# Performance work log

Hardware: AMD Instinct MI355X
Metric: run time of the kernel (lower is better)

## Reference

```python
import jax, jax.numpy as jnp
import numpy as np

N_ATOMS = 512
N_FEATURES = 64
BATCH = 8
BINS = 64
SEG_LEN = 1
LEAKY_SLOPE = 0.01


def _segments(n, length=1):
    # all pairs of segments (i,i+length),(j,j+length), i<j, excluding end1==start2
    n_seg = n - length
    i, j = np.triu_indices(n_seg, k=1)
    seg = np.stack([i, i + length, j, j + length], axis=1)
    return seg[seg[:, 1] != seg[:, 2]].astype(np.int32)


def _nnorm(v):
    return v / jnp.linalg.norm(v, axis=-1, keepdims=True)


def _writhe(segments, xyz):
    # segments: (P,4) int, xyz: (B,N,3) -> (B,P)
    smat = xyz[:, segments]                                  # (B,P,4,3)
    B, P = smat.shape[0], smat.shape[1]
    # displacements r02,r03,r12,r13 (point a in seg1 -> point b in seg2)
    disp = _nnorm((smat[:, :, None, 2:, :] - smat[:, :, :2, None, :]).reshape(B, P, 4, 3))
    idx_a = jnp.array([0, 1, 3, 2])
    idx_b = jnp.array([1, 3, 2, 0])
    crosses = _nnorm(jnp.cross(disp[:, :, idx_a], disp[:, :, idx_b]))
    dots = jnp.clip(jnp.sum(crosses * crosses[:, :, idx_b], axis=-1), -1.0, 1.0)
    omega = jnp.arcsin(dots).sum(-1)                         # (B,P)
    signs = jnp.sign(jnp.sum(
        jnp.cross(_nnorm(smat[:, :, 3] - smat[:, :, 2]), _nnorm(smat[:, :, 1] - smat[:, :, 0]))
        * disp[:, :, 0], axis=-1))
    return omega * signs / (2.0 * jnp.pi)


def _rbf(x, start=-1.0, end=1.0, number=BINS):
    # soft_one_hot_linspace, basis='gaussian', cutoff=False
    values = jnp.linspace(start, end, number, dtype=x.dtype)
    step = values[1] - values[0]
    diff = (x[..., None] - values) / step
    return jnp.exp(-(diff ** 2)) / 1.12


def setup_inputs() -> dict:
    key = jax.random.key(0)
    k = jax.random.split(key, 4)
    seg = jnp.asarray(_segments(N_ATOMS, SEG_LEN))           # (129795,4)
    return {
        "x": jax.random.normal(k[0], (BATCH, N_ATOMS, N_FEATURES), jnp.float32),
        "xyz": jax.random.normal(k[1], (BATCH, N_ATOMS, 3), jnp.float32) * 3.0,
        "segments": seg,
        "W1": jax.random.normal(k[2], (BINS, N_FEATURES), jnp.float32) / np.sqrt(BINS),
        "b1": jnp.zeros((N_FEATURES,), jnp.float32),
        "W2": jax.random.normal(k[3], (N_FEATURES, N_FEATURES), jnp.float32) / np.sqrt(N_FEATURES),
        "b2": jnp.zeros((N_FEATURES,), jnp.float32),
    }


def reference(x, xyz, segments, W1, b1, W2, b2):
    wr = _writhe(segments, xyz)                              # (B,P)
    # bidirectional edges between segment start points
    src = jnp.concatenate([segments[:, 0], segments[:, 2]])  # (E,)
    dst = jnp.concatenate([segments[:, 2], segments[:, 0]])  # (E,)
    wr_e = jnp.concatenate([wr, wr], axis=1)                 # (B,E)
    h = jax.nn.leaky_relu(_rbf(wr_e) @ W1 + b1, LEAKY_SLOPE) # (B,E,F)
    msg = (h @ W2 + b2) * x[:, src]                          # (B,E,F)
    agg = jax.vmap(lambda m: jax.ops.segment_sum(m, dst, num_segments=N_ATOMS))(msg)
    return x + agg                                           # residual update (B,N,F)
```

## Files before the change

### kernel.cpp

```cpp
#include <hip/hip_runtime.h>
#include <hip/hip_bf16.h>
#include <math.h>
#include <stdint.h>

#define N_ATOMS 512
#define NF 64
#define NB 8
#define NBINS 64
#define NSEG 511
#define NTF 8192
#define NSENT 2554
#define ETILES2 254

__device__ __forceinline__ float dot3(float ax, float ay, float az,
                                      float bx, float by, float bz) {
    return fmaf(ax, bx, fmaf(ay, by, az * bz));
}

__device__ __forceinline__ uint16_t bf16_bits(float f) {
    union { __hip_bfloat16 h; uint16_t u; } cv;
    cv.h = __float2bfloat16(f);
    return cv.u;
}

__device__ __forceinline__ float compute_wr(const float* pb, int i, int j) {
    float p0x = pb[3*i+0], p0y = pb[3*i+1], p0z = pb[3*i+2];
    float p1x = pb[3*i+3], p1y = pb[3*i+4], p1z = pb[3*i+5];
    float p2x = pb[3*j+0], p2y = pb[3*j+1], p2z = pb[3*j+2];
    float p3x = pb[3*j+3], p3y = pb[3*j+4], p3z = pb[3*j+5];

    float d0x = p2x-p0x, d0y = p2y-p0y, d0z = p2z-p0z;
    float d1x = p3x-p0x, d1y = p3y-p0y, d1z = p3z-p0z;
    float d2x = p2x-p1x, d2y = p2y-p1y, d2z = p2z-p1z;
    float d3x = p3x-p1x, d3y = p3y-p1y, d3z = p3z-p1z;
    {
        float n0 = rsqrtf(dot3(d0x,d0y,d0z,d0x,d0y,d0z)); d0x*=n0; d0y*=n0; d0z*=n0;
        float n1 = rsqrtf(dot3(d1x,d1y,d1z,d1x,d1y,d1z)); d1x*=n1; d1y*=n1; d1z*=n1;
        float n2 = rsqrtf(dot3(d2x,d2y,d2z,d2x,d2y,d2z)); d2x*=n2; d2y*=n2; d2z*=n2;
        float n3 = rsqrtf(dot3(d3x,d3y,d3z,d3x,d3y,d3z)); d3x*=n3; d3y*=n3; d3z*=n3;
    }
    float c0x = d0y*d1z - d0z*d1y, c0y = d0z*d1x - d0x*d1z, c0z = d0x*d1y - d0y*d1x;
    float c1x = d1y*d3z - d1z*d3y, c1y = d1z*d3x - d1x*d3z, c1z = d1x*d3y - d1y*d3x;
    float c3x = d2y*d0z - d2z*d0y, c3y = d2z*d0x - d2x*d0z, c3z = d2x*d0y - d2y*d0x;
    {
        float n0 = rsqrtf(dot3(c0x,c0y,c0z,c0x,c0y,c0z)); c0x*=n0; c0y*=n0; c0z*=n0;
        float n1 = rsqrtf(dot3(c1x,c1y,c1z,c1x,c1y,c1z)); c1x*=n1; c1y*=n1; c1z*=n1;
        float n3 = rsqrtf(dot3(c3x,c3y,c3z,c3x,c3y,c3z)); c3x*=n3; c3y*=n3; c3z*=n3;
    }
    float t0 = fminf(fmaxf(dot3(c0x,c0y,c0z, c1x,c1y,c1z), -1.f), 1.f);
    float t1 = fminf(fmaxf(dot3(c1x,c1y,c1z, c3x,c3y,c3z), -1.f), 1.f);
    float t3 = fminf(fmaxf(dot3(c3x,c3y,c3z, c0x,c0y,c0z), -1.f), 1.f);
    float omega = asinf(t0) + asinf(t1) + asinf(t3) + 1.5707963267948966f;
    float ex = p3x-p2x, ey = p3y-p2y, ez = p3z-p2z;
    float fx = p1x-p0x, fy = p1y-p0y, fz = p1z-p0z;
    float gx = ey*fz - ez*fy, gy = ez*fx - ex*fz, gz = ex*fy - ey*fx;
    float sgd = dot3(gx,gy,gz, d0x,d0y,d0z);
    float sgn = (sgd > 0.f) ? 1.f : ((sgd < 0.f) ? -1.f : 0.f);
    return omega * sgn * 0.15915494309189535f;
}

__device__ __forceinline__ uint32_t wr_to_off(float w) {
    float tf = (w + 1.0f) * ((float)(NTF - 1) * 0.5f);
    tf = fminf(fmaxf(tf, 0.0f), (float)(NTF - 1));
    int t0 = (int)(tf + 0.5f);
    t0 = (t0 > NTF - 1) ? (NTF - 1) : t0;
    return (uint32_t)t0 << 6;
}

__launch_bounds__(256)
__global__ void prepass(
        const float* __restrict__ xyz, const int* __restrict__ seg,
        const float* __restrict__ W1, const float* __restrict__ b1,
        const float* __restrict__ W2, const float* __restrict__ b2,
        uint16_t* __restrict__ tabh, uint32_t* __restrict__ ta, int P) {
    __shared__ float lds[1536];

    const unsigned bx = blockIdx.x;

    if (bx < NTF / 8) {
        const int widx = threadIdx.x >> 6;
        const int lane = threadIdx.x & 63;
        const int g = bx * 4 + widx;
        const int g2 = g + NTF / 2;

        float tta = ((-1.0f + (2.0f / (float)(NTF - 1)) * (float)g)  + 1.0f) * 31.5f;
        float ttb = ((-1.0f + (2.0f / (float)(NTF - 1)) * (float)g2) + 1.0f) * 31.5f;

        float a0=0.f,a1=0.f,a2=0.f,a3=0.f, e0=0.f,e1=0.f,e2=0.f,e3=0.f;
        #pragma unroll
        for (int k = 0; k < NBINS; k += 4) {
            #pragma unroll
            for (int q = 0; q < 4; ++q) {
                float da = tta - (float)(k + q);
                float db = ttb - (float)(k + q);
                float ra = __expf(-da * da) * 0.8928571428571429f;
                float rb = __expf(-db * db) * 0.8928571428571429f;
                float wv = W1[(k + q) * NF + lane];
                if (q == 0) { a0 = fmaf(ra, wv, a0); e0 = fmaf(rb, wv, e0); }
                if (q == 1) { a1 = fmaf(ra, wv, a1); e1 = fmaf(rb, wv, e1); }
                if (q == 2) { a2 = fmaf(ra, wv, a2); e2 = fmaf(rb, wv, e2); }
                if (q == 3) { a3 = fmaf(ra, wv, a3); e3 = fmaf(rb, wv, e3); }
            }
        }
        float ha = ((a0 + a1) + (a2 + a3)) + b1[lane];
        float hb = ((e0 + e1) + (e2 + e3)) + b1[lane];
        ha = fmaxf(ha, 0.01f * ha);
        hb = fmaxf(hb, 0.01f * hb);
        lds[widx * 64 + lane]       = ha;
        lds[256 + widx * 64 + lane] = hb;
        __syncthreads();

        float m0=0.f,m1=0.f,m2=0.f,m3=0.f, n0=0.f,n1=0.f,n2=0.f,n3=0.f;
        #pragma unroll
        for (int k = 0; k < NF; k += 4) {
            float w0 = W2[(k + 0) * NF + lane];
            float w1v = W2[(k + 1) * NF + lane];
            float w2v = W2[(k + 2) * NF + lane];
            float w3 = W2[(k + 3) * NF + lane];
            m0 = fmaf(lds[widx * 64 + k + 0], w0, m0);
            m1 = fmaf(lds[widx * 64 + k + 1], w1v, m1);
            m2 = fmaf(lds[widx * 64 + k + 2], w2v, m2);
            m3 = fmaf(lds[widx * 64 + k + 3], w3, m3);
            n0 = fmaf(lds[256 + widx * 64 + k + 0], w0, n0);
            n1 = fmaf(lds[256 + widx * 64 + k + 1], w1v, n1);
            n2 = fmaf(lds[256 + widx * 64 + k + 2], w2v, n2);
            n3 = fmaf(lds[256 + widx * 64 + k + 3], w3, n3);
        }
        float ma = ((m0 + m1) + (m2 + m3)) + b2[lane];
        float mb = ((n0 + n1) + (n2 + n3)) + b2[lane];
        tabh[g  * NF + lane] = bf16_bits(ma);
        tabh[g2 * NF + lane] = bf16_bits(mb);
        if (g == 0) tabh[NTF * NF + lane] = 0;
    } else if (bx < NTF / 8 + NB * ETILES2) {
        const int rel = bx - NTF / 8;
        const int b = rel / ETILES2;
        const int tile = rel - b * ETILES2;

        const float* xb = xyz + b * (N_ATOMS * 3);
        #pragma unroll
        for (int k = 0; k < 6; ++k)
            lds[k * 256 + threadIdx.x] = xb[k * 256 + threadIdx.x];
        __syncthreads();

        #pragma unroll
        for (int q = 0; q < 2; ++q) {
            const int e = tile * 512 + q * 256 + threadIdx.x;
            if (e < P) {
                int4 sv = ((const int4*)seg)[e];
                const int i = sv.x;
                const int j = sv.z;
                uint32_t u = wr_to_off(compute_wr(lds, i, j));
                ta[(b << 18) + (i << 9) + j] = u;
                ta[(b << 18) + (j << 9) + i] = u;
            }
        }
    } else {
        const int idx = (bx - (NTF / 8 + NB * ETILES2)) * 256 + threadIdx.x;
        if (idx < NB * NSENT) {
            const int b = idx / NSENT;
            const int k = idx - b * NSENT;
            int d, s;
            if      (k < 512)  { d = k;        s = k;     }
            else if (k < 1023) { d = k - 512;  s = d + 1; }
            else if (k < 1534) { s = k - 1023; d = s + 1; }
            else if (k < 2044) { d = k - 1534; s = NSEG;  }
            else               { s = k - 2044; d = NSEG;  }
            ta[(b << 18) + (d << 9) + s] = (uint32_t)NTF << 6;
        }
    }
}

__launch_bounds__(512)
__global__ void agg11(
        const float* __restrict__ x, const uint32_t* __restrict__ ta,
        const uint16_t* __restrict__ tabh, float* __restrict__ out) {
    __shared__ float xs[8192];

    const int widx = threadIdx.x >> 6;
    const int lane = threadIdx.x & 63;
    const int bid  = blockIdx.x;
    const int b    = bid >> 6;
    const int dst  = ((bid & 63) << 3) + widx;

    const float* xb = x + ((size_t)b << 15);
    const uint32_t* tarow = ta + ((size_t)b << 18) + ((size_t)dst << 9);

    #pragma unroll
    for (int k = 0; k < 8; ++k)
        xs[k * 512 + threadIdx.x] = xb[k * 512 + threadIdx.x];

    float acc = 0.0f;
    for (int c = 0; c < 8; ++c) {
        const int tavc = (int)tarow[(c << 6) + lane];

        __syncthreads();

        if (c < 7) {
            const float* xsrc = xb + ((c + 1) << 12);
            float* xdst = xs + (((c + 1) & 1) << 12);
            #pragma unroll
            for (int k = 0; k < 8; ++k)
                xdst[k * 512 + threadIdx.x] = xsrc[k * 512 + threadIdx.x];
        }

        const float* xc = xs + ((c & 1) << 12) + lane;
        #pragma unroll
        for (int ee = 0; ee < 64; ++ee) {
            const int off = __builtin_amdgcn_readlane(tavc, ee);
            const float mv = __uint_as_float((uint32_t)tabh[off + lane] << 16);
            acc = fmaf(mv, xc[ee << 6], acc);
        }
    }

    out[((size_t)b << 15) + (dst << 6) + lane] = xb[(dst << 6) + lane] + acc;
}


__global__ void init_out_kernel(const float* __restrict__ x, float* __restrict__ out, int n) {
    int idx = blockIdx.x * blockDim.x + threadIdx.x;
    if (idx < n) out[idx] = x[idx];
}

__device__ __forceinline__ void compute_m(
        const float* __restrict__ pb, int i, int j,
        const float* __restrict__ W1, const float* __restrict__ b1,
        const float* __restrict__ W2, const float* __restrict__ b2,
        float* __restrict__ mout) {
    float wr = compute_wr(pb, i, j);
    float acc_[NBINS];
    {
        float tt = (wr + 1.0f) * 31.5f;
        #pragma unroll
        for (int k = 0; k < NBINS; ++k) {
            float d = tt - (float)k;
            acc_[k] = __expf(-d * d) * 0.8928571428571429f;
        }
    }
    float h_[NF];
    #pragma unroll
    for (int f = 0; f < NF; ++f) h_[f] = b1[f];
    #pragma unroll
    for (int k = 0; k < NBINS; ++k) {
        float r = acc_[k];
        #pragma unroll
        for (int f = 0; f < NF; ++f) h_[f] = fmaf(r, W1[k * NF + f], h_[f]);
    }
    #pragma unroll
    for (int f = 0; f < NF; ++f) h_[f] = fmaxf(h_[f], 0.01f * h_[f]);
    #pragma unroll
    for (int f = 0; f < NF; ++f) acc_[f] = b2[f];
    #pragma unroll
    for (int k = 0; k < NF; ++k) {
        float hk = h_[k];
        #pragma unroll
        for (int f = 0; f < NF; ++f) acc_[f] = fmaf(hk, W2[k * NF + f], acc_[f]);
    }
    #pragma unroll
    for (int f = 0; f < NF; ++f) mout[f] = acc_[f];
}

__launch_bounds__(256, 2)
__global__ void writhe_msg_atomic_kernel(
        const float* __restrict__ x, const float* __restrict__ xyz,
        const int* __restrict__ seg,
        const float* __restrict__ W1, const float* __restrict__ b1,
        const float* __restrict__ W2, const float* __restrict__ b2,
        float* __restrict__ out, int P, int n_tiles) {
    __shared__ __hip_bfloat16 lds_m[4][64 * 65];
    __shared__ int lds_i[4][64];
    __shared__ int lds_j[4][64];

    const int widx = threadIdx.x >> 6;
    const int lane = threadIdx.x & 63;
    const int wave_g = blockIdx.x * 4 + widx;
    const int b = wave_g / n_tiles;
    const int tile = wave_g - b * n_tiles;
    const int bc = (b < NB) ? b : 0;
    const int e = tile * 64 + lane;
    const bool valid = (b < NB) && (e < P);

    int4 sv = valid ? ((const int4*)seg)[e] : make_int4(0, 1, 2, 3);
    const int i = sv.x;
    const int j = sv.z;

    float m[NF];
    compute_m(xyz + bc * (N_ATOMS * 3), i, j, W1, b1, W2, b2, m);

    const float scale = valid ? 1.0f : 0.0f;
    #pragma unroll
    for (int f = 0; f < NF; ++f)
        lds_m[widx][lane * 65 + f] = __float2bfloat16(m[f] * scale);
    lds_i[widx][lane] = i;
    lds_j[widx][lane] = j;
    __syncthreads();

    const float* xb = x + bc * (N_ATOMS * NF);
    float* ob = out + bc * (N_ATOMS * NF);
    int cur_i = lds_i[widx][0];
    float acc_i = 0.0f;
    for (int ee = 0; ee < 64; ++ee) {
        int ie = lds_i[widx][ee];
        int je = lds_j[widx][ee];
        float mv = __bfloat162float(lds_m[widx][ee * 65 + lane]);
        float xi = xb[ie * NF + lane];
        float xj = xb[je * NF + lane];
        atomicAdd(&ob[je * NF + lane], mv * xi);
        if (ie != cur_i) {
            atomicAdd(&ob[cur_i * NF + lane], acc_i);
            acc_i = 0.0f;
            cur_i = ie;
        }
        acc_i = fmaf(mv, xj, acc_i);
    }
    atomicAdd(&ob[cur_i * NF + lane], acc_i);
}

extern "C" void kernel_launch(void* const* d_in, const int* in_sizes, int n_in,
                              void* d_out, int out_size, void* d_ws, size_t ws_size,
                              hipStream_t stream) {
    const float* x   = (const float*)d_in[0];
    const float* xyz = (const float*)d_in[1];
    const int*   seg = (const int*)d_in[2];
    const float* W1  = (const float*)d_in[3];
    const float* b1  = (const float*)d_in[4];
    const float* W2  = (const float*)d_in[5];
    const float* b2  = (const float*)d_in[6];
    float* out = (float*)d_out;

    const int P = in_sizes[2] / 4;
    const int n_tiles = (P + 63) / 64;

    const size_t tabh_bytes = (size_t)(NTF + 1) * NF * sizeof(uint16_t);
    const size_t ta_bytes   = (size_t)NB * N_ATOMS * N_ATOMS * sizeof(uint32_t);
    const size_t need_ws = tabh_bytes + ta_bytes;

    if (ws_size >= need_ws && P <= ETILES2 * 512) {
        uint16_t* tabh = (uint16_t*)d_ws;
        uint32_t* ta   = (uint32_t*)((char*)d_ws + tabh_bytes);

        const int nsent_blocks = (NB * NSENT + 255) / 256;
        const int total_blocks = NTF / 8 + NB * ETILES2 + nsent_blocks;
        hipLaunchKernelGGL(prepass, dim3(total_blocks), dim3(256), 0, stream,
                           xyz, seg, W1, b1, W2, b2, tabh, ta, P);

        hipLaunchKernelGGL(agg11, dim3(NB * 64), dim3(512), 0, stream,
                           x, ta, tabh, out);
    } else {
        const int n = out_size;
        hipLaunchKernelGGL(init_out_kernel, dim3((n + 255) / 256), dim3(256), 0, stream,
                           x, out, n);
        const int total_waves = NB * n_tiles;
        const int blocks = (total_waves + 3) / 4;
        hipLaunchKernelGGL(writhe_msg_atomic_kernel, dim3(blocks), dim3(256), 0, stream,
                           x, xyz, seg, W1, b1, W2, b2, out, P, n_tiles);
    }
}
```

Measured before the change: 117.6 us.

## Split aggregation source range across two wave groups per block with shared-memory reduction

```diff
diff --git a/kernel.cpp b/kernel.cpp
--- a/kernel.cpp
+++ b/kernel.cpp
@@ -170,40 +170,50 @@
     }
 }
 
-__launch_bounds__(512)
-__global__ void agg11(
+__launch_bounds__(1024, 8)
+__global__ void agg12(
         const float* __restrict__ x, const uint32_t* __restrict__ ta,
         const uint16_t* __restrict__ tabh, float* __restrict__ out) {
-    __shared__ float xs[8192];
-
-    const int widx = threadIdx.x >> 6;
-    const int lane = threadIdx.x & 63;
+    __shared__ float xs[16384];
+
+    const int tid  = threadIdx.x;
+    const int widx = tid >> 6;
+    const int lane = tid & 63;
+    const int h    = widx >> 3;
+    const int r    = widx & 7;
+    const int ht   = tid & 511;
     const int bid  = blockIdx.x;
     const int b    = bid >> 6;
-    const int dst  = ((bid & 63) << 3) + widx;
+    const int dst  = ((bid & 63) << 3) + r;
 
     const float* xb = x + ((size_t)b << 15);
     const uint32_t* tarow = ta + ((size_t)b << 18) + ((size_t)dst << 9);
 
-    #pragma unroll
-    for (int k = 0; k < 8; ++k)
-        xs[k * 512 + threadIdx.x] = xb[k * 512 + threadIdx.x];
+    {
+        const float* xsrc = xb + ((h * 4) << 12);
+        float* xdst = xs + (h << 12);
+        #pragma unroll
+        for (int k = 0; k < 8; ++k)
+            xdst[k * 512 + ht] = xsrc[k * 512 + ht];
+    }
 
     float acc = 0.0f;
-    for (int c = 0; c < 8; ++c) {
+    #pragma unroll
+    for (int p = 0; p < 4; ++p) {
+        const int c = h * 4 + p;
         const int tavc = (int)tarow[(c << 6) + lane];
 
         __syncthreads();
 
-        if (c < 7) {
+        if (p < 3) {
             const float* xsrc = xb + ((c + 1) << 12);
-            float* xdst = xs + (((c + 1) & 1) << 12);
+            float* xdst = xs + ((((p + 1) & 1) << 13) + (h << 12));
             #pragma unroll
             for (int k = 0; k < 8; ++k)
-                xdst[k * 512 + threadIdx.x] = xsrc[k * 512 + threadIdx.x];
-        }
-
-        const float* xc = xs + ((c & 1) << 12) + lane;
+                xdst[k * 512 + ht] = xsrc[k * 512 + ht];
+        }
+
+        const float* xc = xs + (((p & 1) << 13) + (h << 12)) + lane;
         #pragma unroll
         for (int ee = 0; ee < 64; ++ee) {
             const int off = __builtin_amdgcn_readlane(tavc, ee);
@@ -212,7 +222,12 @@
         }
     }
 
-    out[((size_t)b << 15) + (dst << 6) + lane] = xb[(dst << 6) + lane] + acc;
+    __syncthreads();
+    if (h == 1) xs[(r << 6) + lane] = acc;
+    __syncthreads();
+    if (h == 0)
+        out[((size_t)b << 15) + (dst << 6) + lane] =
+            xb[(dst << 6) + lane] + acc + xs[(r << 6) + lane];
 }
 
 
@@ -343,7 +358,7 @@
         hipLaunchKernelGGL(prepass, dim3(total_blocks), dim3(256), 0, stream,
                            xyz, seg, W1, b1, W2, b2, tabh, ta, P);
 
-        hipLaunchKernelGGL(agg11, dim3(NB * 64), dim3(512), 0, stream,
+        hipLaunchKernelGGL(agg12, dim3(NB * 64), dim3(1024), 0, stream,
                            x, ta, tabh, out);
     } else {
         const int n = out_size;
```

New measurement: 134.9 us. 14.7% more time.
